# Performance work log

Measured on AMD Instinct MI355X. Metric: run time of the kernel, lower is better.

## Reference

```python
import jax, jax.numpy as jnp
import numpy as np

B, T, E = 4, 2048, 1024
H, D = 16, 64  # n_heads, head_size


def setup_inputs() -> dict:
    key = jax.random.key(0)
    ks = jax.random.split(key, 6)
    s = 0.02
    x = jax.random.normal(ks[0], (B, T, E), dtype=jnp.float32)
    Wq = jax.random.normal(ks[1], (H, E, D), dtype=jnp.float32) * s
    Wk = jax.random.normal(ks[2], (H, E, D), dtype=jnp.float32) * s
    Wv = jax.random.normal(ks[3], (H, E, D), dtype=jnp.float32) * s
    Wp = jax.random.normal(ks[4], (E, E), dtype=jnp.float32) * s
    bp = jnp.zeros((E,), dtype=jnp.float32)
    return {"x": x, "Wq": Wq, "Wk": Wk, "Wv": Wv, "Wp": Wp, "bp": bp}


def reference(x, Wq, Wk, Wv, Wp, bp):
    # Per-head bias-free Q/K/V projections (vectorized over heads)
    q = jnp.einsum('bte,hed->bhtd', x, Wq)
    k = jnp.einsum('bte,hed->bhtd', x, Wk)
    v = jnp.einsum('bte,hed->bhtd', x, Wv)
    scale = 1.0 / jnp.sqrt(jnp.asarray(D, dtype=x.dtype))
    scores = jnp.einsum('bhtd,bhsd->bhts', q, k) * scale  # [B,H,T,T]
    causal = jnp.tril(jnp.ones((T, T), dtype=bool))
    scores = jnp.where(causal, scores, jnp.asarray(-jnp.inf, dtype=scores.dtype))
    attn = jax.nn.softmax(scores, axis=-1)
    out = jnp.einsum('bhts,bhsd->bhtd', attn, v)  # [B,H,T,D]
    # concat heads: 'nh b t c -> b t (nh c)'
    out = out.transpose(0, 2, 1, 3).reshape(B, T, H * D)
    # output projection (dropout p=0.0 is identity)
    return out @ Wp.T + bp
```

## Files before the change

kernel.cpp:

```cpp
#include <hip/hip_runtime.h>

typedef unsigned short u16;
typedef __attribute__((ext_vector_type(8))) short bf16x8;
typedef __attribute__((ext_vector_type(4))) short bf16x4;
typedef __attribute__((ext_vector_type(4))) float f32x4;

__device__ __forceinline__ u16 f2bf(float f) {
  unsigned u = __float_as_uint(f);
  u += 0x7FFFu + ((u >> 16) & 1u);
  return (u16)(u >> 16);
}
__device__ __forceinline__ unsigned pack2(float a, float b) {
  return (unsigned)f2bf(a) | ((unsigned)f2bf(b) << 16);
}
__device__ __forceinline__ uint4 pack8(float4 a, float4 b) {
  uint4 r;
  r.x = pack2(a.x, a.y); r.y = pack2(a.z, a.w);
  r.z = pack2(b.x, b.y); r.w = pack2(b.z, b.w);
  return r;
}
__device__ __forceinline__ void gload16(const void* g, void* l) {
  __builtin_amdgcn_global_load_lds(
      (const __attribute__((address_space(1))) void*)g,
      (__attribute__((address_space(3))) void*)l, 16, 0, 0);
}
__device__ __forceinline__ f32x4 mfma16(bf16x4 a, bf16x4 b, f32x4 c) {
#if __has_builtin(__builtin_amdgcn_mfma_f32_16x16x16bf16_1k)
  return __builtin_amdgcn_mfma_f32_16x16x16bf16_1k(a, b, c, 0, 0, 0);
#elif __has_builtin(__builtin_amdgcn_mfma_f32_16x16x16_bf16)
  return __builtin_amdgcn_mfma_f32_16x16x16_bf16(a, b, c, 0, 0, 0);
#else
  asm volatile("v_mfma_f32_16x16x16_bf16 %0, %1, %2, %0\n\ts_nop 2"
               : "+v"(c) : "v"(a), "v"(b));
  return c;
#endif
}

__global__ __launch_bounds__(256) void prep(
    const float* __restrict__ x, u16* __restrict__ xbf,
    const float* __restrict__ Wq, const float* __restrict__ Wk,
    const float* __restrict__ Wv, u16* __restrict__ wt,
    const float* __restrict__ Wp, u16* __restrict__ wpbf) {
  const int tid = threadIdx.x;
  const int b = blockIdx.x;
  __shared__ __align__(16) u16 tile[64 * 72];
  if (b < 4096) {
    const size_t i = (size_t)b * 256 + tid;
    const float4* p = (const float4*)(x + i * 8);
    *(uint4*)(xbf + i * 8) = pack8(p[0], p[1]);
  } else if (b < 4864) {
    const int idx = b - 4096;
    const int w = idx >> 8;
    const int mat = (idx >> 4) & 15;
    const int r0 = (idx & 15) * 64;
    const float* src = (w == 0 ? Wq : (w == 1 ? Wk : Wv)) + (size_t)mat * 1024 * 64;
    u16* dst = wt + (size_t)w * 1024 * 1024 + (size_t)mat * 1024 * 64;
#pragma unroll
    for (int i = 0; i < 2; ++i) {
      const int c = tid + i * 256;
      const int r = c >> 3, off = (c & 7) * 8;
      const float* p = src + (size_t)(r0 + r) * 64 + off;
      *(uint4*)(&tile[r * 72 + off]) = pack8(*(const float4*)p, *(const float4*)(p + 4));
    }
    __syncthreads();
#pragma unroll
    for (int i = 0; i < 2; ++i) {
      const int c = tid + i * 256;
      const int d = c >> 3, roff = (c & 7) * 8;
      bf16x8 v;
#pragma unroll
      for (int j = 0; j < 8; ++j) v[j] = (short)tile[(roff + j) * 72 + d];
      *(bf16x8*)(dst + (size_t)d * 1024 + r0 + roff) = v;
    }
  } else {
    const size_t i = (size_t)(b - 4864) * 256 + tid;
    const float4* p = (const float4*)(Wp + i * 8);
    *(uint4*)(wpbf + i * 8) = pack8(p[0], p[1]);
  }
}

template <int MODE>
__global__ __launch_bounds__(256) void gemm_bt(
    const u16* __restrict__ A, const u16* __restrict__ BT,
    u16* __restrict__ o0, u16* __restrict__ o1, u16* __restrict__ o2,
    float* __restrict__ fout, const float* __restrict__ bp) {
  __shared__ __align__(16) u16 As[128 * 32];
  __shared__ __align__(16) u16 Bs[128 * 32];
  const int tid = threadIdx.x;
  const int lane = tid & 63, wv = tid >> 6;
  const int g = lane >> 4, ln = lane & 15;
  const int wm = wv >> 1, wn = wv & 1;
  const int m0 = blockIdx.x * 128, n0 = blockIdx.y * 128;

  const f32x4 fz = {0.f, 0.f, 0.f, 0.f};
  f32x4 acc[4][4];
#pragma unroll
  for (int i = 0; i < 4; ++i)
#pragma unroll
    for (int j = 0; j < 4; ++j) acc[i][j] = fz;

  for (int k0 = 0; k0 < 1024; k0 += 32) {
    __syncthreads();
#pragma unroll
    for (int i = 0; i < 2; ++i) {
      const int c = tid + i * 256;
      const int r = c >> 2, off = (c & 3) * 8;
      gload16(A + (size_t)(m0 + r) * 1024 + k0 + off, &As[c * 8]);
      gload16(BT + (size_t)(n0 + r) * 1024 + k0 + off, &Bs[c * 8]);
    }
    __syncthreads();
    bf16x8 af[4], bfr[4];
#pragma unroll
    for (int rt = 0; rt < 4; ++rt)
      af[rt] = *(const bf16x8*)(&As[(wm * 64 + rt * 16 + ln) * 32 + g * 8]);
#pragma unroll
    for (int ct = 0; ct < 4; ++ct)
      bfr[ct] = *(const bf16x8*)(&Bs[(wn * 64 + ct * 16 + ln) * 32 + g * 8]);
#pragma unroll
    for (int rt = 0; rt < 4; ++rt)
#pragma unroll
      for (int ct = 0; ct < 4; ++ct)
        acc[rt][ct] = __builtin_amdgcn_mfma_f32_16x16x32_bf16(af[rt], bfr[ct],
                                                              acc[rt][ct], 0, 0, 0);
  }

  if (MODE == 0) {
    const int which = n0 >> 10;
    const int nl0 = (n0 & 1023) + wn * 64;
    const float qs = (which == 0) ? 0.1803368801f : 1.0f;
    if (which < 2) {
      u16* outp = which == 0 ? o0 : o1;
#pragma unroll
      for (int rt = 0; rt < 4; ++rt)
#pragma unroll
        for (int ct = 0; ct < 4; ++ct) {
          const int nl = nl0 + ct * 16 + ln;
          const int h = nl >> 6, d = nl & 63;
#pragma unroll
          for (int r = 0; r < 4; ++r) {
            const int m = m0 + wm * 64 + rt * 16 + 4 * g + r;
            const int b = m >> 11, t = m & 2047;
            outp[(((size_t)(b * 16 + h) * 2048 + t) << 6) + d] =
                f2bf(acc[rt][ct][r] * qs);
          }
        }
    } else {
#pragma unroll
      for (int rt = 0; rt < 4; ++rt) {
        const int tb = m0 + wm * 64 + rt * 16 + 4 * g;
        const int b = tb >> 11, t = tb & 2047;
#pragma unroll
        for (int ct = 0; ct < 4; ++ct) {
          const int nl = nl0 + ct * 16 + ln;
          const int h = nl >> 6, d = nl & 63;
          u16* dst = o2 + ((size_t)((b * 16 + h) * 64 + d) << 11) + t;
#pragma unroll
          for (int r = 0; r < 4; ++r) dst[r] = f2bf(acc[rt][ct][r]);
        }
      }
    }
  } else {
#pragma unroll
    for (int ct = 0; ct < 4; ++ct) {
      const int n = n0 + wn * 64 + ct * 16 + ln;
      const float bias = bp[n];
#pragma unroll
      for (int rt = 0; rt < 4; ++rt)
#pragma unroll
        for (int r = 0; r < 4; ++r) {
          const int m = m0 + wm * 64 + rt * 16 + 4 * g + r;
          fout[(size_t)m * 1024 + n] = acc[rt][ct][r] + bias;
        }
    }
  }
}

__global__ __launch_bounds__(256) void attn_kernel(
    const u16* __restrict__ Q, const u16* __restrict__ K,
    const u16* __restrict__ VT, u16* __restrict__ AO) {
  const int tid = threadIdx.x;
  const int wv = tid >> 6, lane = tid & 63, g = lane >> 4, ln = lane & 15;
  const int bh = blockIdx.x;
  const int qi = 15 - (int)blockIdx.y;
  const int q0 = qi * 128;
  const int nt = 2 * qi + 2;
  const int ntw = 2 * qi + 1 + (wv >> 1);
  const u16* Qb = Q + (size_t)bh * (2048 * 64);
  const u16* Kb = K + (size_t)bh * (2048 * 64);
  const u16* Vb = VT + (size_t)bh * (64 * 2048);

  __shared__ __align__(16) u16 Ks[64 * 72];
  __shared__ __align__(16) u16 Vs[64 * 72];

  const int sr0 = tid >> 3, so0 = (tid & 7) * 8;
  const int sr1 = (tid + 256) >> 3, so1 = ((tid + 256) & 7) * 8;

  uint4 kpf0 = *(const uint4*)(Kb + (size_t)sr0 * 64 + so0);
  uint4 kpf1 = *(const uint4*)(Kb + (size_t)sr1 * 64 + so1);
  uint4 vpf0 = *(const uint4*)(Vb + (size_t)sr0 * 2048 + so0);
  uint4 vpf1 = *(const uint4*)(Vb + (size_t)sr1 * 2048 + so1);

  bf16x8 qa[2][2];
#pragma unroll
  for (int rt = 0; rt < 2; ++rt) {
    const int row = q0 + wv * 32 + rt * 16 + ln;
#pragma unroll
    for (int h = 0; h < 2; ++h)
      qa[rt][h] = *(const bf16x8*)(Qb + (size_t)row * 64 + h * 32 + g * 8);
  }

  const f32x4 fz = {0.f, 0.f, 0.f, 0.f};
  f32x4 oacc[2][4], lacc[2];
#pragma unroll
  for (int rt = 0; rt < 2; ++rt) {
    lacc[rt] = fz;
#pragma unroll
    for (int dt = 0; dt < 4; ++dt) oacc[rt][dt] = fz;
  }

  const short ob = 0x3F80;
  const bf16x4 ones = {ob, ob, ob, ob};

  for (int kt = 0; kt < nt; ++kt) {
    __syncthreads();
    *(uint4*)(&Ks[sr0 * 72 + so0]) = kpf0;
    *(uint4*)(&Ks[sr1 * 72 + so1]) = kpf1;
    *(uint4*)(&Vs[sr0 * 72 + so0]) = vpf0;
    *(uint4*)(&Vs[sr1 * 72 + so1]) = vpf1;
    __syncthreads();
    if (kt + 1 < nt) {
      const int sn = (kt + 1) * 64;
      kpf0 = *(const uint4*)(Kb + (size_t)(sn + sr0) * 64 + so0);
      kpf1 = *(const uint4*)(Kb + (size_t)(sn + sr1) * 64 + so1);
      vpf0 = *(const uint4*)(Vb + (size_t)sr0 * 2048 + sn + so0);
      vpf1 = *(const uint4*)(Vb + (size_t)sr1 * 2048 + sn + so1);
    }
    if (kt < ntw) {
      const int s0 = kt * 64;
      f32x4 sfT[2][4];
#pragma unroll
      for (int rt = 0; rt < 2; ++rt)
#pragma unroll
        for (int st = 0; st < 4; ++st) sfT[rt][st] = fz;
#pragma unroll
      for (int st = 0; st < 4; ++st) {
        const bf16x8 kb0 = *(const bf16x8*)(&Ks[(st * 16 + ln) * 72 + g * 8]);
        const bf16x8 kb1 = *(const bf16x8*)(&Ks[(st * 16 + ln) * 72 + 32 + g * 8]);
#pragma unroll
        for (int rt = 0; rt < 2; ++rt) {
          sfT[rt][st] = __builtin_amdgcn_mfma_f32_16x16x32_bf16(kb0, qa[rt][0],
                                                                sfT[rt][st], 0, 0, 0);
          sfT[rt][st] = __builtin_amdgcn_mfma_f32_16x16x32_bf16(kb1, qa[rt][1],
                                                                sfT[rt][st], 0, 0, 0);
        }
      }
      const bool diag = (kt == ntw - 1);
      bf16x4 pa[2][4];
#pragma unroll
      for (int rt = 0; rt < 2; ++rt) {
        const int qg = q0 + wv * 32 + rt * 16 + ln;
#pragma unroll
        for (int st = 0; st < 4; ++st) {
          const int sb = s0 + st * 16 + 4 * g;
#pragma unroll
          for (int r = 0; r < 4; ++r) {
            float e = __builtin_amdgcn_exp2f(sfT[rt][st][r]);
            if (diag && (sb + r > qg)) e = 0.f;
            pa[rt][st][r] = (short)f2bf(e);
          }
        }
      }
#pragma unroll
      for (int st = 0; st < 4; ++st) {
#pragma unroll
        for (int dt = 0; dt < 4; ++dt) {
          const bf16x4 vb =
              *(const bf16x4*)(&Vs[(dt * 16 + ln) * 72 + st * 16 + 4 * g]);
#pragma unroll
          for (int rt = 0; rt < 2; ++rt)
            oacc[rt][dt] = mfma16(pa[rt][st], vb, oacc[rt][dt]);
        }
#pragma unroll
        for (int rt = 0; rt < 2; ++rt)
          lacc[rt] = mfma16(pa[rt][st], ones, lacc[rt]);
      }
    }
  }

  const int b = bh >> 4, h = bh & 15;
#pragma unroll
  for (int rt = 0; rt < 2; ++rt) {
    float linv[4];
#pragma unroll
    for (int r = 0; r < 4; ++r) linv[r] = 1.f / lacc[rt][r];
#pragma unroll
    for (int dt = 0; dt < 4; ++dt)
#pragma unroll
      for (int r = 0; r < 4; ++r) {
        const int qg = q0 + wv * 32 + rt * 16 + 4 * g + r;
        AO[(size_t)(b * 2048 + qg) * 1024 + h * 64 + dt * 16 + ln] =
            f2bf(oacc[rt][dt][r] * linv[r]);
      }
  }
}

extern "C" void kernel_launch(void* const* d_in, const int* in_sizes, int n_in,
                              void* d_out, int out_size, void* d_ws, size_t ws_size,
                              hipStream_t stream) {
  const float* x  = (const float*)d_in[0];
  const float* Wq = (const float*)d_in[1];
  const float* Wk = (const float*)d_in[2];
  const float* Wv = (const float*)d_in[3];
  const float* Wp = (const float*)d_in[4];
  const float* bp = (const float*)d_in[5];
  float* out = (float*)d_out;

  char* ws = (char*)d_ws;
  const size_t MB = 1048576;
  u16* xbf  = (u16*)(ws);
  u16* aows = (u16*)(ws);
  u16* wt   = (u16*)(ws + 16 * MB);
  u16* wpbf = (u16*)(ws + 22 * MB);
  u16* qws  = (u16*)(ws + 24 * MB - 2 * MB + 2 * MB);
  qws  = (u16*)(ws + 24 * MB - 2 * MB);
  qws  = (u16*)(ws + 24 * MB);
  u16* kws  = (u16*)(ws + 40 * MB);
  u16* vtws = (u16*)(ws + 56 * MB);

  prep<<<dim3(5376), 256, 0, stream>>>(x, xbf, Wq, Wk, Wv, wt, Wp, wpbf);
  gemm_bt<0><<<dim3(64, 24), 256, 0, stream>>>(xbf, wt, qws, kws, vtws,
                                               nullptr, nullptr);
  attn_kernel<<<dim3(64, 16), 256, 0, stream>>>(qws, kws, vtws, aows);
  gemm_bt<1><<<dim3(64, 8), 256, 0, stream>>>(aows, wpbf, nullptr, nullptr,
                                              nullptr, out, bp);
}
```

Measured before the change: 273.5 us.

## Pair causal query tiles per block for balanced attention work

Each attention block now handles two 64-row query tiles, tile jb and tile 31-jb, so every block does the same total number of key tiles. This replaces the earlier 128-row tiles, where the last warps idled on the diagonal and blocks were unevenly loaded. Each wave now holds one 16-row tile instead of two, which halves the MFMA work per K/V tile load. It also switches bf16 packing to a hardware cvt_pk builtin when one is available. The cost is more K/V loads to shared memory per query row, since each tile is now 64 rows instead of 128.

```diff
diff --git a/kernel.cpp b/kernel.cpp
--- a/kernel.cpp
+++ b/kernel.cpp
@@ -13,6 +13,15 @@
 __device__ __forceinline__ unsigned pack2(float a, float b) {
   return (unsigned)f2bf(a) | ((unsigned)f2bf(b) << 16);
 }
+#if __has_builtin(__builtin_amdgcn_cvt_pk_bf16_f32)
+typedef __attribute__((ext_vector_type(2))) __bf16 bf16v2;
+__device__ __forceinline__ unsigned cvt_pk(float a, float b) {
+  bf16v2 v = __builtin_amdgcn_cvt_pk_bf16_f32(a, b);
+  return __builtin_bit_cast(unsigned, v);
+}
+#else
+__device__ __forceinline__ unsigned cvt_pk(float a, float b) { return pack2(a, b); }
+#endif
 __device__ __forceinline__ uint4 pack8(float4 a, float4 b) {
   uint4 r;
   r.x = pack2(a.x, a.y); r.y = pack2(a.z, a.w);
@@ -181,10 +190,7 @@
   const int tid = threadIdx.x;
   const int wv = tid >> 6, lane = tid & 63, g = lane >> 4, ln = lane & 15;
   const int bh = blockIdx.x;
-  const int qi = 15 - (int)blockIdx.y;
-  const int q0 = qi * 128;
-  const int nt = 2 * qi + 2;
-  const int ntw = 2 * qi + 1 + (wv >> 1);
+  const int jb = blockIdx.y;
   const u16* Qb = Q + (size_t)bh * (2048 * 64);
   const u16* Kb = K + (size_t)bh * (2048 * 64);
   const u16* Vb = VT + (size_t)bh * (64 * 2048);
@@ -193,82 +199,70 @@
   __shared__ __align__(16) u16 Vs[64 * 72];
 
   const int sr0 = tid >> 3, so0 = (tid & 7) * 8;
-  const int sr1 = (tid + 256) >> 3, so1 = ((tid + 256) & 7) * 8;
+  const int sr1 = sr0 + 32;
 
   uint4 kpf0 = *(const uint4*)(Kb + (size_t)sr0 * 64 + so0);
-  uint4 kpf1 = *(const uint4*)(Kb + (size_t)sr1 * 64 + so1);
+  uint4 kpf1 = *(const uint4*)(Kb + (size_t)sr1 * 64 + so0);
   uint4 vpf0 = *(const uint4*)(Vb + (size_t)sr0 * 2048 + so0);
-  uint4 vpf1 = *(const uint4*)(Vb + (size_t)sr1 * 2048 + so1);
-
-  bf16x8 qa[2][2];
-#pragma unroll
-  for (int rt = 0; rt < 2; ++rt) {
-    const int row = q0 + wv * 32 + rt * 16 + ln;
-#pragma unroll
-    for (int h = 0; h < 2; ++h)
-      qa[rt][h] = *(const bf16x8*)(Qb + (size_t)row * 64 + h * 32 + g * 8);
-  }
-
-  const f32x4 fz = {0.f, 0.f, 0.f, 0.f};
-  f32x4 oacc[2][4], lacc[2];
-#pragma unroll
-  for (int rt = 0; rt < 2; ++rt) {
-    lacc[rt] = fz;
-#pragma unroll
-    for (int dt = 0; dt < 4; ++dt) oacc[rt][dt] = fz;
-  }
-
+  uint4 vpf1 = *(const uint4*)(Vb + (size_t)sr1 * 2048 + so0);
+
+  const int b = bh >> 4, h = bh & 15;
   const short ob = 0x3F80;
   const bf16x4 ones = {ob, ob, ob, ob};
-
-  for (int kt = 0; kt < nt; ++kt) {
-    __syncthreads();
-    *(uint4*)(&Ks[sr0 * 72 + so0]) = kpf0;
-    *(uint4*)(&Ks[sr1 * 72 + so1]) = kpf1;
-    *(uint4*)(&Vs[sr0 * 72 + so0]) = vpf0;
-    *(uint4*)(&Vs[sr1 * 72 + so1]) = vpf1;
-    __syncthreads();
-    if (kt + 1 < nt) {
-      const int sn = (kt + 1) * 64;
-      kpf0 = *(const uint4*)(Kb + (size_t)(sn + sr0) * 64 + so0);
-      kpf1 = *(const uint4*)(Kb + (size_t)(sn + sr1) * 64 + so1);
-      vpf0 = *(const uint4*)(Vb + (size_t)sr0 * 2048 + sn + so0);
-      vpf1 = *(const uint4*)(Vb + (size_t)sr1 * 2048 + sn + so1);
-    }
-    if (kt < ntw) {
-      const int s0 = kt * 64;
-      f32x4 sfT[2][4];
-#pragma unroll
-      for (int rt = 0; rt < 2; ++rt)
-#pragma unroll
-        for (int st = 0; st < 4; ++st) sfT[rt][st] = fz;
+  const f32x4 fz = {0.f, 0.f, 0.f, 0.f};
+
+#pragma unroll
+  for (int ph = 0; ph < 2; ++ph) {
+    const int qi = (ph == 0) ? jb : 31 - jb;
+    const int q0 = qi * 64;
+    const int nt = qi + 1;
+    const int qrow = q0 + wv * 16 + ln;
+    const bf16x8 qa0 = *(const bf16x8*)(Qb + (size_t)qrow * 64 + g * 8);
+    const bf16x8 qa1 = *(const bf16x8*)(Qb + (size_t)qrow * 64 + 32 + g * 8);
+
+    f32x4 oacc[4];
+    f32x4 lacc = fz;
+#pragma unroll
+    for (int dt = 0; dt < 4; ++dt) oacc[dt] = fz;
+
+    for (int kt = 0; kt < nt; ++kt) {
+      __syncthreads();
+      *(uint4*)(&Ks[sr0 * 72 + so0]) = kpf0;
+      *(uint4*)(&Ks[sr1 * 72 + so0]) = kpf1;
+      *(uint4*)(&Vs[sr0 * 72 + so0]) = vpf0;
+      *(uint4*)(&Vs[sr1 * 72 + so0]) = vpf1;
+      __syncthreads();
+      if ((kt + 1 < nt) || (ph == 0)) {
+        const int sn = (kt + 1 < nt) ? (kt + 1) * 64 : 0;
+        kpf0 = *(const uint4*)(Kb + (size_t)(sn + sr0) * 64 + so0);
+        kpf1 = *(const uint4*)(Kb + (size_t)(sn + sr1) * 64 + so0);
+        vpf0 = *(const uint4*)(Vb + (size_t)sr0 * 2048 + sn + so0);
+        vpf1 = *(const uint4*)(Vb + (size_t)sr1 * 2048 + sn + so0);
+      }
+      f32x4 sfT[4];
+#pragma unroll
+      for (int st = 0; st < 4; ++st) sfT[st] = fz;
 #pragma unroll
       for (int st = 0; st < 4; ++st) {
         const bf16x8 kb0 = *(const bf16x8*)(&Ks[(st * 16 + ln) * 72 + g * 8]);
         const bf16x8 kb1 = *(const bf16x8*)(&Ks[(st * 16 + ln) * 72 + 32 + g * 8]);
-#pragma unroll
-        for (int rt = 0; rt < 2; ++rt) {
-          sfT[rt][st] = __builtin_amdgcn_mfma_f32_16x16x32_bf16(kb0, qa[rt][0],
-                                                                sfT[rt][st], 0, 0, 0);
-          sfT[rt][st] = __builtin_amdgcn_mfma_f32_16x16x32_bf16(kb1, qa[rt][1],
-                                                                sfT[rt][st], 0, 0, 0);
-        }
-      }
-      const bool diag = (kt == ntw - 1);
-      bf16x4 pa[2][4];
-#pragma unroll
-      for (int rt = 0; rt < 2; ++rt) {
-        const int qg = q0 + wv * 32 + rt * 16 + ln;
-#pragma unroll
-        for (int st = 0; st < 4; ++st) {
-          const int sb = s0 + st * 16 + 4 * g;
-#pragma unroll
-          for (int r = 0; r < 4; ++r) {
-            float e = __builtin_amdgcn_exp2f(sfT[rt][st][r]);
-            if (diag && (sb + r > qg)) e = 0.f;
-            pa[rt][st][r] = (short)f2bf(e);
-          }
-        }
+        sfT[st] = __builtin_amdgcn_mfma_f32_16x16x32_bf16(kb0, qa0, sfT[st], 0, 0, 0);
+        sfT[st] = __builtin_amdgcn_mfma_f32_16x16x32_bf16(kb1, qa1, sfT[st], 0, 0, 0);
+      }
+      const bool diag = (kt == nt - 1);
+      bf16x4 pa[4];
+#pragma unroll
+      for (int st = 0; st < 4; ++st) {
+        float e[4];
+#pragma unroll
+        for (int r = 0; r < 4; ++r) e[r] = __builtin_amdgcn_exp2f(sfT[st][r]);
+        if (diag) {
+#pragma unroll
+          for (int r = 0; r < 4; ++r)
+            if (st * 16 + 4 * g + r > wv * 16 + ln) e[r] = 0.f;
+        }
+        uint2 packed = {cvt_pk(e[0], e[1]), cvt_pk(e[2], e[3])};
+        pa[st] = __builtin_bit_cast(bf16x4, packed);
       }
 #pragma unroll
       for (int st = 0; st < 4; ++st) {
@@ -276,30 +270,21 @@
         for (int dt = 0; dt < 4; ++dt) {
           const bf16x4 vb =
               *(const bf16x4*)(&Vs[(dt * 16 + ln) * 72 + st * 16 + 4 * g]);
-#pragma unroll
-          for (int rt = 0; rt < 2; ++rt)
-            oacc[rt][dt] = mfma16(pa[rt][st], vb, oacc[rt][dt]);
-        }
-#pragma unroll
-        for (int rt = 0; rt < 2; ++rt)
-          lacc[rt] = mfma16(pa[rt][st], ones, lacc[rt]);
-      }
-    }
-  }
-
-  const int b = bh >> 4, h = bh & 15;
-#pragma unroll
-  for (int rt = 0; rt < 2; ++rt) {
+          oacc[dt] = mfma16(pa[st], vb, oacc[dt]);
+        }
+        lacc = mfma16(pa[st], ones, lacc);
+      }
+    }
     float linv[4];
 #pragma unroll
-    for (int r = 0; r < 4; ++r) linv[r] = 1.f / lacc[rt][r];
+    for (int r = 0; r < 4; ++r) linv[r] = 1.f / lacc[r];
 #pragma unroll
     for (int dt = 0; dt < 4; ++dt)
 #pragma unroll
       for (int r = 0; r < 4; ++r) {
-        const int qg = q0 + wv * 32 + rt * 16 + 4 * g + r;
+        const int qg = q0 + wv * 16 + 4 * g + r;
         AO[(size_t)(b * 2048 + qg) * 1024 + h * 64 + dt * 16 + ln] =
-            f2bf(oacc[rt][dt][r] * linv[r]);
+            f2bf(oacc[dt][r] * linv[r]);
       }
   }
 }
@@ -321,9 +306,7 @@
   u16* aows = (u16*)(ws);
   u16* wt   = (u16*)(ws + 16 * MB);
   u16* wpbf = (u16*)(ws + 22 * MB);
-  u16* qws  = (u16*)(ws + 24 * MB - 2 * MB + 2 * MB);
-  qws  = (u16*)(ws + 24 * MB - 2 * MB);
-  qws  = (u16*)(ws + 24 * MB);
+  u16* qws  = (u16*)(ws + 24 * MB);
   u16* kws  = (u16*)(ws + 40 * MB);
   u16* vtws = (u16*)(ws + 56 * MB);
 
```

After: 274.1 us. Within noise of the previous version (+0.2%).

## Pair causal query tiles per attention block and use packed bf16 conversion

Applied to the files above, without the earlier changes.

Each attention block now handles two query tiles, jb and 15-jb, one after the other, so every block does the same total causal work. The grid is halved to 64x8. This removes load imbalance and the tail effect from very unequal tiles. The K/V prefetch at the end of the first phase reloads tile 0 so the second phase can start right away. The exp-to-bf16 conversion now uses the hardware packed cvt instruction when available, and the diagonal mask is computed with local indices. The trade-off is fewer blocks in flight (512), which may lower occupancy and latency hiding.

```diff
diff --git a/kernel.cpp b/kernel.cpp
--- a/kernel.cpp
+++ b/kernel.cpp
@@ -13,6 +13,15 @@
 __device__ __forceinline__ unsigned pack2(float a, float b) {
   return (unsigned)f2bf(a) | ((unsigned)f2bf(b) << 16);
 }
+#if __has_builtin(__builtin_amdgcn_cvt_pk_bf16_f32)
+typedef __attribute__((ext_vector_type(2))) __bf16 bf16v2;
+__device__ __forceinline__ unsigned cvt_pk(float a, float b) {
+  bf16v2 v = __builtin_amdgcn_cvt_pk_bf16_f32(a, b);
+  return __builtin_bit_cast(unsigned, v);
+}
+#else
+__device__ __forceinline__ unsigned cvt_pk(float a, float b) { return pack2(a, b); }
+#endif
 __device__ __forceinline__ uint4 pack8(float4 a, float4 b) {
   uint4 r;
   r.x = pack2(a.x, a.y); r.y = pack2(a.z, a.w);
@@ -181,10 +190,7 @@
   const int tid = threadIdx.x;
   const int wv = tid >> 6, lane = tid & 63, g = lane >> 4, ln = lane & 15;
   const int bh = blockIdx.x;
-  const int qi = 15 - (int)blockIdx.y;
-  const int q0 = qi * 128;
-  const int nt = 2 * qi + 2;
-  const int ntw = 2 * qi + 1 + (wv >> 1);
+  const int jb = blockIdx.y;
   const u16* Qb = Q + (size_t)bh * (2048 * 64);
   const u16* Kb = K + (size_t)bh * (2048 * 64);
   const u16* Vb = VT + (size_t)bh * (64 * 2048);
@@ -193,114 +199,125 @@
   __shared__ __align__(16) u16 Vs[64 * 72];
 
   const int sr0 = tid >> 3, so0 = (tid & 7) * 8;
-  const int sr1 = (tid + 256) >> 3, so1 = ((tid + 256) & 7) * 8;
+  const int sr1 = sr0 + 32;
 
   uint4 kpf0 = *(const uint4*)(Kb + (size_t)sr0 * 64 + so0);
-  uint4 kpf1 = *(const uint4*)(Kb + (size_t)sr1 * 64 + so1);
+  uint4 kpf1 = *(const uint4*)(Kb + (size_t)sr1 * 64 + so0);
   uint4 vpf0 = *(const uint4*)(Vb + (size_t)sr0 * 2048 + so0);
-  uint4 vpf1 = *(const uint4*)(Vb + (size_t)sr1 * 2048 + so1);
-
-  bf16x8 qa[2][2];
-#pragma unroll
-  for (int rt = 0; rt < 2; ++rt) {
-    const int row = q0 + wv * 32 + rt * 16 + ln;
-#pragma unroll
-    for (int h = 0; h < 2; ++h)
-      qa[rt][h] = *(const bf16x8*)(Qb + (size_t)row * 64 + h * 32 + g * 8);
-  }
-
-  const f32x4 fz = {0.f, 0.f, 0.f, 0.f};
-  f32x4 oacc[2][4], lacc[2];
-#pragma unroll
-  for (int rt = 0; rt < 2; ++rt) {
-    lacc[rt] = fz;
-#pragma unroll
-    for (int dt = 0; dt < 4; ++dt) oacc[rt][dt] = fz;
-  }
-
+  uint4 vpf1 = *(const uint4*)(Vb + (size_t)sr1 * 2048 + so0);
+
+  const int b = bh >> 4, h = bh & 15;
   const short ob = 0x3F80;
   const bf16x4 ones = {ob, ob, ob, ob};
-
-  for (int kt = 0; kt < nt; ++kt) {
-    __syncthreads();
-    *(uint4*)(&Ks[sr0 * 72 + so0]) = kpf0;
-    *(uint4*)(&Ks[sr1 * 72 + so1]) = kpf1;
-    *(uint4*)(&Vs[sr0 * 72 + so0]) = vpf0;
-    *(uint4*)(&Vs[sr1 * 72 + so1]) = vpf1;
-    __syncthreads();
-    if (kt + 1 < nt) {
-      const int sn = (kt + 1) * 64;
-      kpf0 = *(const uint4*)(Kb + (size_t)(sn + sr0) * 64 + so0);
-      kpf1 = *(const uint4*)(Kb + (size_t)(sn + sr1) * 64 + so1);
-      vpf0 = *(const uint4*)(Vb + (size_t)sr0 * 2048 + sn + so0);
-      vpf1 = *(const uint4*)(Vb + (size_t)sr1 * 2048 + sn + so1);
-    }
-    if (kt < ntw) {
-      const int s0 = kt * 64;
-      f32x4 sfT[2][4];
-#pragma unroll
-      for (int rt = 0; rt < 2; ++rt)
-#pragma unroll
-        for (int st = 0; st < 4; ++st) sfT[rt][st] = fz;
-#pragma unroll
-      for (int st = 0; st < 4; ++st) {
-        const bf16x8 kb0 = *(const bf16x8*)(&Ks[(st * 16 + ln) * 72 + g * 8]);
-        const bf16x8 kb1 = *(const bf16x8*)(&Ks[(st * 16 + ln) * 72 + 32 + g * 8]);
+  const f32x4 fz = {0.f, 0.f, 0.f, 0.f};
+
+#pragma unroll
+  for (int ph = 0; ph < 2; ++ph) {
+    const int qi = (ph == 0) ? jb : 15 - jb;
+    const int q0 = qi * 128;
+    const int nt = 2 * qi + 2;
+    const int ntw = 2 * qi + 1 + (wv >> 1);
+
+    bf16x8 qa[2][2];
+#pragma unroll
+    for (int rt = 0; rt < 2; ++rt) {
+      const int row = q0 + wv * 32 + rt * 16 + ln;
+#pragma unroll
+      for (int hh = 0; hh < 2; ++hh)
+        qa[rt][hh] = *(const bf16x8*)(Qb + (size_t)row * 64 + hh * 32 + g * 8);
+    }
+
+    f32x4 oacc[2][4], lacc[2];
+#pragma unroll
+    for (int rt = 0; rt < 2; ++rt) {
+      lacc[rt] = fz;
+#pragma unroll
+      for (int dt = 0; dt < 4; ++dt) oacc[rt][dt] = fz;
+    }
+
+    for (int kt = 0; kt < nt; ++kt) {
+      __syncthreads();
+      *(uint4*)(&Ks[sr0 * 72 + so0]) = kpf0;
+      *(uint4*)(&Ks[sr1 * 72 + so0]) = kpf1;
+      *(uint4*)(&Vs[sr0 * 72 + so0]) = vpf0;
+      *(uint4*)(&Vs[sr1 * 72 + so0]) = vpf1;
+      __syncthreads();
+      if ((kt + 1 < nt) || (ph == 0)) {
+        const int sn = (kt + 1 < nt) ? (kt + 1) * 64 : 0;
+        kpf0 = *(const uint4*)(Kb + (size_t)(sn + sr0) * 64 + so0);
+        kpf1 = *(const uint4*)(Kb + (size_t)(sn + sr1) * 64 + so0);
+        vpf0 = *(const uint4*)(Vb + (size_t)sr0 * 2048 + sn + so0);
+        vpf1 = *(const uint4*)(Vb + (size_t)sr1 * 2048 + sn + so0);
+      }
+      if (kt < ntw) {
+        const int s0 = kt * 64;
+        f32x4 sfT[2][4];
+#pragma unroll
+        for (int rt = 0; rt < 2; ++rt)
+#pragma unroll
+          for (int st = 0; st < 4; ++st) sfT[rt][st] = fz;
+#pragma unroll
+        for (int st = 0; st < 4; ++st) {
+          const bf16x8 kb0 = *(const bf16x8*)(&Ks[(st * 16 + ln) * 72 + g * 8]);
+          const bf16x8 kb1 = *(const bf16x8*)(&Ks[(st * 16 + ln) * 72 + 32 + g * 8]);
+#pragma unroll
+          for (int rt = 0; rt < 2; ++rt) {
+            sfT[rt][st] = __builtin_amdgcn_mfma_f32_16x16x32_bf16(kb0, qa[rt][0],
+                                                                  sfT[rt][st], 0, 0, 0);
+            sfT[rt][st] = __builtin_amdgcn_mfma_f32_16x16x32_bf16(kb1, qa[rt][1],
+                                                                  sfT[rt][st], 0, 0, 0);
+          }
+        }
+        const bool diag = (kt == ntw - 1);
+        bf16x4 pa[2][4];
 #pragma unroll
         for (int rt = 0; rt < 2; ++rt) {
-          sfT[rt][st] = __builtin_amdgcn_mfma_f32_16x16x32_bf16(kb0, qa[rt][0],
-                                                                sfT[rt][st], 0, 0, 0);
-          sfT[rt][st] = __builtin_amdgcn_mfma_f32_16x16x32_bf16(kb1, qa[rt][1],
-                                                                sfT[rt][st], 0, 0, 0);
+          const int qloc = wv * 32 + rt * 16 + ln;
+#pragma unroll
+          for (int st = 0; st < 4; ++st) {
+            float e[4];
+#pragma unroll
+            for (int r = 0; r < 4; ++r) e[r] = __builtin_amdgcn_exp2f(sfT[rt][st][r]);
+            if (diag) {
+              const int sloc = s0 - q0 + st * 16 + 4 * g;
+#pragma unroll
+              for (int r = 0; r < 4; ++r)
+                if (sloc + r > qloc) e[r] = 0.f;
+            }
+            uint2 packed = {cvt_pk(e[0], e[1]), cvt_pk(e[2], e[3])};
+            pa[rt][st] = __builtin_bit_cast(bf16x4, packed);
+          }
+        }
+#pragma unroll
+        for (int st = 0; st < 4; ++st) {
+#pragma unroll
+          for (int dt = 0; dt < 4; ++dt) {
+            const bf16x4 vb =
+                *(const bf16x4*)(&Vs[(dt * 16 + ln) * 72 + st * 16 + 4 * g]);
+#pragma unroll
+            for (int rt = 0; rt < 2; ++rt)
+              oacc[rt][dt] = mfma16(pa[rt][st], vb, oacc[rt][dt]);
+          }
+#pragma unroll
+          for (int rt = 0; rt < 2; ++rt)
+            lacc[rt] = mfma16(pa[rt][st], ones, lacc[rt]);
         }
       }
-      const bool diag = (kt == ntw - 1);
-      bf16x4 pa[2][4];
-#pragma unroll
-      for (int rt = 0; rt < 2; ++rt) {
-        const int qg = q0 + wv * 32 + rt * 16 + ln;
-#pragma unroll
-        for (int st = 0; st < 4; ++st) {
-          const int sb = s0 + st * 16 + 4 * g;
-#pragma unroll
-          for (int r = 0; r < 4; ++r) {
-            float e = __builtin_amdgcn_exp2f(sfT[rt][st][r]);
-            if (diag && (sb + r > qg)) e = 0.f;
-            pa[rt][st][r] = (short)f2bf(e);
-          }
-        }
-      }
-#pragma unroll
-      for (int st = 0; st < 4; ++st) {
-#pragma unroll
-        for (int dt = 0; dt < 4; ++dt) {
-          const bf16x4 vb =
-              *(const bf16x4*)(&Vs[(dt * 16 + ln) * 72 + st * 16 + 4 * g]);
-#pragma unroll
-          for (int rt = 0; rt < 2; ++rt)
-            oacc[rt][dt] = mfma16(pa[rt][st], vb, oacc[rt][dt]);
-        }
-#pragma unroll
-        for (int rt = 0; rt < 2; ++rt)
-          lacc[rt] = mfma16(pa[rt][st], ones, lacc[rt]);
-      }
-    }
-  }
-
-  const int b = bh >> 4, h = bh & 15;
-#pragma unroll
-  for (int rt = 0; rt < 2; ++rt) {
-    float linv[4];
-#pragma unroll
-    for (int r = 0; r < 4; ++r) linv[r] = 1.f / lacc[rt][r];
-#pragma unroll
-    for (int dt = 0; dt < 4; ++dt)
-#pragma unroll
-      for (int r = 0; r < 4; ++r) {
-        const int qg = q0 + wv * 32 + rt * 16 + 4 * g + r;
-        AO[(size_t)(b * 2048 + qg) * 1024 + h * 64 + dt * 16 + ln] =
-            f2bf(oacc[rt][dt][r] * linv[r]);
-      }
+    }
+#pragma unroll
+    for (int rt = 0; rt < 2; ++rt) {
+      float linv[4];
+#pragma unroll
+      for (int r = 0; r < 4; ++r) linv[r] = 1.f / lacc[rt][r];
+#pragma unroll
+      for (int dt = 0; dt < 4; ++dt)
+#pragma unroll
+        for (int r = 0; r < 4; ++r) {
+          const int qg = q0 + wv * 32 + rt * 16 + 4 * g + r;
+          AO[(size_t)(b * 2048 + qg) * 1024 + h * 64 + dt * 16 + ln] =
+              f2bf(oacc[rt][dt][r] * linv[r]);
+        }
+    }
   }
 }
 
@@ -321,16 +338,14 @@
   u16* aows = (u16*)(ws);
   u16* wt   = (u16*)(ws + 16 * MB);
   u16* wpbf = (u16*)(ws + 22 * MB);
-  u16* qws  = (u16*)(ws + 24 * MB - 2 * MB + 2 * MB);
-  qws  = (u16*)(ws + 24 * MB - 2 * MB);
-  qws  = (u16*)(ws + 24 * MB);
+  u16* qws  = (u16*)(ws + 24 * MB);
   u16* kws  = (u16*)(ws + 40 * MB);
   u16* vtws = (u16*)(ws + 56 * MB);
 
   prep<<<dim3(5376), 256, 0, stream>>>(x, xbf, Wq, Wk, Wv, wt, Wp, wpbf);
   gemm_bt<0><<<dim3(64, 24), 256, 0, stream>>>(xbf, wt, qws, kws, vtws,
                                                nullptr, nullptr);
-  attn_kernel<<<dim3(64, 16), 256, 0, stream>>>(qws, kws, vtws, aows);
+  attn_kernel<<<dim3(64, 8), 256, 0, stream>>>(qws, kws, vtws, aows);
   gemm_bt<1><<<dim3(64, 8), 256, 0, stream>>>(aows, wpbf, nullptr, nullptr,
                                               nullptr, out, bp);
 }
```

Result: no change. 268.2 us (-1.9%).
